# Optimization experiments

Measured on AMD Instinct MI355X. Metric: run time of the kernel, lower is better.

The kernel has to match this reference:

```python
import jax, jax.numpy as jnp
import numpy as np


def setup_inputs() -> dict:
    key = jax.random.key(0)
    inputs = jax.random.normal(key, (64, 2048, 512), dtype=jnp.float32)
    return {"inputs": inputs}


def reference(inputs) -> jnp.ndarray:
    # l2_type == 'one_by_one': squared L2 distance between consecutive timesteps,
    # with a leading 0, normalized per-sequence by the max distance.
    x = inputs.astype(jnp.float32)
    diffs = x[:, 1:] - x[:, :-1]                      # [B, S-1, D]
    d = jnp.sum(diffs * diffs, axis=-1)               # [B, S-1]
    B = x.shape[0]
    d = jnp.concatenate([jnp.zeros((B, 1), d.dtype), d], axis=1)  # [B, S]
    d = d / jnp.max(d, axis=1, keepdims=True)         # normalize by per-seq max
    return d
```

## Files before the change

kernel.cpp:

```cpp
#include <hip/hip_runtime.h>

#define NB 64
#define NS 2048
#define ND 512
#define K  32
#define WPB 4
#define GPB (NS / K / WPB)
#define NRUN (NS / K)

__global__ __launch_bounds__(256, 4) void l2_dist_kernel(const float* __restrict__ x,
                                                         float* __restrict__ out,
                                                         float* __restrict__ runmax) {
    const int b    = blockIdx.y;
    const int wave = threadIdx.x >> 6;
    const int lane = threadIdx.x & 63;
    const int g    = blockIdx.x * WPB + wave;
    const int s0   = g * K;

    const float4* xb = (const float4*)(x + (size_t)b * NS * ND);
    const int RW = ND / 4;
    const int c0 = lane * 2;

    const int sp = (s0 > 0) ? s0 - 1 : 0;
    float4 p0 = xb[(size_t)sp * RW + c0];
    float4 p1 = xb[(size_t)sp * RW + c0 + 1];

    float wmax = 0.0f;

    #pragma unroll 4
    for (int i = 0; i < K; ++i) {
        const int s = s0 + i;
        float4 c0v = xb[(size_t)s * RW + c0];
        float4 c1v = xb[(size_t)s * RW + c0 + 1];
        float dx, sum = 0.0f;
        dx = c0v.x - p0.x; sum += dx * dx;
        dx = c0v.y - p0.y; sum += dx * dx;
        dx = c0v.z - p0.z; sum += dx * dx;
        dx = c0v.w - p0.w; sum += dx * dx;
        dx = c1v.x - p1.x; sum += dx * dx;
        dx = c1v.y - p1.y; sum += dx * dx;
        dx = c1v.z - p1.z; sum += dx * dx;
        dx = c1v.w - p1.w; sum += dx * dx;
        p0 = c0v; p1 = c1v;
        #pragma unroll
        for (int m = 32; m >= 1; m >>= 1)
            sum += __shfl_xor(sum, m, 64);
        if (lane == 0) out[(size_t)b * NS + s] = sum;
        wmax = fmaxf(wmax, sum);
    }

    if (lane == 0) runmax[b * NRUN + g] = wmax;
}

__global__ __launch_bounds__(256) void l2_norm_kernel(float* __restrict__ out,
                                                      const float* __restrict__ runmax) {
    const int b    = blockIdx.y;
    const int half = blockIdx.x;
    const int tid  = threadIdx.x;

    __shared__ float smax;
    if (tid < 64) {
        float v = runmax[b * NRUN + tid];
        #pragma unroll
        for (int m = 32; m >= 1; m >>= 1)
            v = fmaxf(v, __shfl_xor(v, m, 64));
        if (tid == 0) smax = v;
    }
    __syncthreads();
    const float inv = 1.0f / smax;

    float4* row = (float4*)(out + (size_t)b * NS) + half * 256 + tid;
    float4 v = *row;
    v.x *= inv; v.y *= inv; v.z *= inv; v.w *= inv;
    *row = v;
}

extern "C" void kernel_launch(void* const* d_in, const int* in_sizes, int n_in,
                              void* d_out, int out_size, void* d_ws, size_t ws_size,
                              hipStream_t stream) {
    const float* x = (const float*)d_in[0];
    float* out     = (float*)d_out;
    float* runmax  = (float*)d_ws;

    l2_dist_kernel<<<dim3(GPB, NB), dim3(256), 0, stream>>>(x, out, runmax);
    l2_norm_kernel<<<dim3(2, NB), dim3(256), 0, stream>>>(out, runmax);
}
```

Before: 355.8 us.

## Halve rows per wave, coalesce loads, prefetch next row, batch output stores

Each wave now handles 16 timesteps instead of 32, which doubles the number of waves and raises the occupancy hint to 8. Lanes now load interleaved float4s (lane and lane+64) rather than adjacent pairs, so each wave-wide load is fully contiguous. The next row is loaded one iteration ahead of its use, and per-step distances are kept in lanes and written with a single vectorised store instead of one lane-0 store per step. More groups means more redundant boundary-row reads and twice as many run-max entries, so the norm kernel reduces 128 entries.

```diff
diff --git a/kernel.cpp b/kernel.cpp
--- a/kernel.cpp
+++ b/kernel.cpp
@@ -3,12 +3,13 @@
 #define NB 64
 #define NS 2048
 #define ND 512
-#define K  32
+#define K  16
 #define WPB 4
 #define GPB (NS / K / WPB)
 #define NRUN (NS / K)
+#define RW4 (ND / 4)
 
-__global__ __launch_bounds__(256, 4) void l2_dist_kernel(const float* __restrict__ x,
+__global__ __launch_bounds__(256, 8) void l2_dist_kernel(const float* __restrict__ x,
                                                          float* __restrict__ out,
                                                          float* __restrict__ runmax) {
     const int b    = blockIdx.y;
@@ -17,38 +18,63 @@
     const int g    = blockIdx.x * WPB + wave;
     const int s0   = g * K;
 
-    const float4* xb = (const float4*)(x + (size_t)b * NS * ND);
-    const int RW = ND / 4;
-    const int c0 = lane * 2;
+    const float4* row  = (const float4*)(x + (size_t)b * NS * ND) + (size_t)s0 * RW4 + lane;
+    const float4* prow = (s0 > 0) ? row - RW4 : row;
 
-    const int sp = (s0 > 0) ? s0 - 1 : 0;
-    float4 p0 = xb[(size_t)sp * RW + c0];
-    float4 p1 = xb[(size_t)sp * RW + c0 + 1];
+    float4 p0 = prow[0];
+    float4 p1 = prow[64];
+    float4 c0 = row[0];
+    float4 c1 = row[64];
 
     float wmax = 0.0f;
+    float myd  = 0.0f;
 
-    #pragma unroll 4
-    for (int i = 0; i < K; ++i) {
-        const int s = s0 + i;
-        float4 c0v = xb[(size_t)s * RW + c0];
-        float4 c1v = xb[(size_t)s * RW + c0 + 1];
+    #pragma unroll 5
+    for (int i = 0; i < K - 1; ++i) {
+        const float4* nrow = row + (size_t)(i + 1) * RW4;
+        float4 n0 = nrow[0];
+        float4 n1 = nrow[64];
+
         float dx, sum = 0.0f;
-        dx = c0v.x - p0.x; sum += dx * dx;
-        dx = c0v.y - p0.y; sum += dx * dx;
-        dx = c0v.z - p0.z; sum += dx * dx;
-        dx = c0v.w - p0.w; sum += dx * dx;
-        dx = c1v.x - p1.x; sum += dx * dx;
-        dx = c1v.y - p1.y; sum += dx * dx;
-        dx = c1v.z - p1.z; sum += dx * dx;
-        dx = c1v.w - p1.w; sum += dx * dx;
-        p0 = c0v; p1 = c1v;
+        dx = c0.x - p0.x; sum += dx * dx;
+        dx = c0.y - p0.y; sum += dx * dx;
+        dx = c0.z - p0.z; sum += dx * dx;
+        dx = c0.w - p0.w; sum += dx * dx;
+        dx = c1.x - p1.x; sum += dx * dx;
+        dx = c1.y - p1.y; sum += dx * dx;
+        dx = c1.z - p1.z; sum += dx * dx;
+        dx = c1.w - p1.w; sum += dx * dx;
+
         #pragma unroll
         for (int m = 32; m >= 1; m >>= 1)
             sum += __shfl_xor(sum, m, 64);
-        if (lane == 0) out[(size_t)b * NS + s] = sum;
+
         wmax = fmaxf(wmax, sum);
+        myd  = (lane == i) ? sum : myd;
+
+        p0 = c0; p1 = c1; c0 = n0; c1 = n1;
     }
 
+    {
+        float dx, sum = 0.0f;
+        dx = c0.x - p0.x; sum += dx * dx;
+        dx = c0.y - p0.y; sum += dx * dx;
+        dx = c0.z - p0.z; sum += dx * dx;
+        dx = c0.w - p0.w; sum += dx * dx;
+        dx = c1.x - p1.x; sum += dx * dx;
+        dx = c1.y - p1.y; sum += dx * dx;
+        dx = c1.z - p1.z; sum += dx * dx;
+        dx = c1.w - p1.w; sum += dx * dx;
+
+        #pragma unroll
+        for (int m = 32; m >= 1; m >>= 1)
+            sum += __shfl_xor(sum, m, 64);
+
+        wmax = fmaxf(wmax, sum);
+        myd  = (lane == K - 1) ? sum : myd;
+    }
+
+    if (lane < K) out[(size_t)b * NS + s0 + lane] = myd;
     if (lane == 0) runmax[b * NRUN + g] = wmax;
 }
 
@@ -60,7 +86,7 @@
 
     __shared__ float smax;
     if (tid < 64) {
-        float v = runmax[b * NRUN + tid];
+        float v = fmaxf(runmax[b * NRUN + tid], runmax[b * NRUN + 64 + tid]);
         #pragma unroll
         for (int m = 32; m >= 1; m >>= 1)
             v = fmaxf(v, __shfl_xor(v, m, 64));
@@ -69,10 +95,10 @@
     __syncthreads();
     const float inv = 1.0f / smax;
 
-    float4* row = (float4*)(out + (size_t)b * NS) + half * 256 + tid;
-    float4 v = *row;
+    float4* rowp = (float4*)(out + (size_t)b * NS) + half * 256 + tid;
+    float4 v = *rowp;
     v.x *= inv; v.y *= inv; v.z *= inv; v.w *= inv;
-    *row = v;
+    *rowp = v;
 }
 
 extern "C" void kernel_launch(void* const* d_in, const int* in_sizes, int n_in,
```

Result: no change. 356.4 us (+0.2%).
